# Kernel optimization log

Measured on AMD Instinct MI355X. Metric: run time of the kernel, lower is better.

Reference implementation:

```python
import jax, jax.numpy as jnp
import numpy as np

B, N, E = 4, 2048, 512
H = 8
HD = E // H  # 64
SCALE = HD ** -0.5


def setup_inputs() -> dict:
    key = jax.random.key(0)
    k1, k2, k3 = jax.random.split(key, 3)
    x = jax.random.normal(k1, (B, N, E), dtype=jnp.float32)
    # xavier-uniform-like scaling for weights
    w_qkv = jax.random.normal(k2, (3 * E, E), dtype=jnp.float32) * (2.0 / (4 * E)) ** 0.5
    b_qkv = jnp.zeros((3 * E,), dtype=jnp.float32)
    w_out = jax.random.normal(k3, (E, E), dtype=jnp.float32) * (1.0 / E) ** 0.5
    b_out = jnp.zeros((E,), dtype=jnp.float32)
    return {"x": x, "w_qkv": w_qkv, "b_qkv": b_qkv, "w_out": w_out, "b_out": b_out}


def reference(x, w_qkv, b_qkv, w_out, b_out):
    b_sz, n_patches, _ = x.shape
    # qkv projection: [B,N,3E] -> [B,N,3,H,HD] -> [B,H,3,N,HD]
    qkv = (jnp.einsum('bne,fe->bnf', x, w_qkv) + b_qkv)
    qkv = qkv.reshape(b_sz, n_patches, 3, H, HD).transpose(0, 3, 2, 1, 4)
    q, k, v = qkv[:, :, 0], qkv[:, :, 1], qkv[:, :, 2]  # each [B,H,N,HD]
    attn = jnp.einsum('bhqd,bhkd->bhqk', q * SCALE, k)  # [B,H,N,N]
    attn = jax.nn.softmax(attn, axis=-1)
    # attn_dropout p=0.0 -> identity in reference
    out = jnp.einsum('bhqk,bhkd->bhqd', attn, v)  # [B,H,N,HD]
    out = out.transpose(0, 2, 1, 3).reshape(b_sz, n_patches, E)
    out = jnp.einsum('bne,fe->bnf', out, w_out) + b_out
    return out
```

## Files before the change

kernel.cpp:

```cpp
#include <hip/hip_runtime.h>

#define BB   4
#define SEQ  2048
#define EMB  512
#define NH   8
#define HD   64
#define QSCALE 0.18033688011f

typedef __bf16 bf16x8 __attribute__((ext_vector_type(8)));
typedef float  f32x4  __attribute__((ext_vector_type(4)));

__device__ __forceinline__ short f2bf(float f) {
  union { float f; unsigned u; } v; v.f = f;
  unsigned r = v.u + 0x7fffu + ((v.u >> 16) & 1u);
  return (short)(r >> 16);
}

__device__ __forceinline__ unsigned pk_bf16(float a, float b) {
#if __has_builtin(__builtin_amdgcn_cvt_pk_bf16_f32)
  typedef __bf16 bf16v2 __attribute__((ext_vector_type(2)));
  union { bf16v2 v; unsigned u; } cv;
  cv.v = __builtin_amdgcn_cvt_pk_bf16_f32(a, b);
  return cv.u;
#else
  return (unsigned)(unsigned short)f2bf(a) | ((unsigned)(unsigned short)f2bf(b) << 16);
#endif
}

__device__ __forceinline__ float fexp2(float x) {
#if __has_builtin(__builtin_amdgcn_exp2f)
  return __builtin_amdgcn_exp2f(x);
#else
  return exp2f(x);
#endif
}

__device__ __forceinline__ void gl_lds16(const void* g, void* l) {
  __builtin_amdgcn_global_load_lds(
      (const __attribute__((address_space(1))) unsigned int*)g,
      (__attribute__((address_space(3))) unsigned int*)l, 16, 0, 0);
}

__device__ __forceinline__ void quad_redist(unsigned &a, unsigned &b) {
  asm volatile("v_permlane32_swap_b32 %0, %1" : "+v"(a), "+v"(b));
  asm volatile("v_permlane16_swap_b32 %0, %1" : "+v"(a), "+v"(b));
}

__global__ __launch_bounds__(256) void cast_all(const float* __restrict__ x,
                                                const float* __restrict__ wq,
                                                const float* __restrict__ wo,
                                                short* __restrict__ xb,
                                                short* __restrict__ wqb,
                                                short* __restrict__ wob) {
  int i = blockIdx.x * 256 + threadIdx.x;
  const float* src; short* dst; int off;
  if (i < 1048576)      { src = x;  dst = xb;  off = i; }
  else if (i < 1245184) { src = wq; dst = wqb; off = i - 1048576; }
  else                  { src = wo; dst = wob; off = i - 1245184; }
  float4 v = ((const float4*)src)[off];
  uint2 o; o.x = pk_bf16(v.x, v.y); o.y = pk_bf16(v.z, v.w);
  *(uint2*)&dst[off * 4] = o;
}

__global__ __launch_bounds__(256) void qkv_gemm(const short* __restrict__ A,
                                                const short* __restrict__ W,
                                                const float* __restrict__ bias,
                                                short* __restrict__ qo,
                                                short* __restrict__ ko,
                                                short* __restrict__ vto) {
  __shared__ __align__(16) short As0[128 * 32];
  __shared__ __align__(16) short Bs0[128 * 32];
  __shared__ __align__(16) short As1[128 * 32];
  __shared__ __align__(16) short Bs1[128 * 32];
  const int tid  = threadIdx.x;
  const int lane = tid & 63, wave = tid >> 6;
  const int wm = wave >> 1, wf = wave & 1;
  const int col = lane & 15, quad = lane >> 4;
  const int m0 = blockIdx.x * 128, f0 = blockIdx.y * 128;

  const short* aSrc[2]; const short* wSrc[2];
#pragma unroll
  for (int rd = 0; rd < 2; ++rd) {
    int slot = rd * 256 + tid;
    int row  = slot >> 2;
    int cb   = (slot & 3) ^ ((slot >> 3) & 3);
    aSrc[rd] = A + (size_t)(m0 + row) * 512 + cb * 8;
    wSrc[rd] = W + (size_t)(f0 + row) * 512 + cb * 8;
  }
  int aOff[4], bOff[4];
  const int rc = (quad ^ ((col >> 1) & 3)) * 8;
#pragma unroll
  for (int i = 0; i < 4; ++i) {
    aOff[i] = (wm * 64 + i * 16 + col) * 32 + rc;
    bOff[i] = (wf * 64 + i * 16 + col) * 32 + rc;
  }

  f32x4 acc[4][4];
#pragma unroll
  for (int i = 0; i < 4; ++i)
#pragma unroll
    for (int j = 0; j < 4; ++j)
#pragma unroll
      for (int r = 0; r < 4; ++r) acc[i][j][r] = 0.f;

#define QSTAGE(BUFA, BUFB, KS)                                         \
  {                                                                    \
    const int ko_ = (KS) * 32;                                         \
    gl_lds16(aSrc[0] + ko_, (char*)(BUFA) + wave * 1024);              \
    gl_lds16(aSrc[1] + ko_, (char*)(BUFA) + 4096 + wave * 1024);       \
    gl_lds16(wSrc[0] + ko_, (char*)(BUFB) + wave * 1024);              \
    gl_lds16(wSrc[1] + ko_, (char*)(BUFB) + 4096 + wave * 1024);       \
  }

  auto qcompute = [&](const short* As, const short* Bs) {
    bf16x8 af[4], bw[4];
#pragma unroll
    for (int i = 0; i < 4; ++i) af[i] = *(const bf16x8*)&As[aOff[i]];
#pragma unroll
    for (int j = 0; j < 4; ++j) bw[j] = *(const bf16x8*)&Bs[bOff[j]];
#pragma unroll
    for (int i = 0; i < 4; ++i)
#pragma unroll
      for (int j = 0; j < 4; ++j)
        acc[i][j] = __builtin_amdgcn_mfma_f32_16x16x32_bf16(af[i], bw[j], acc[i][j], 0, 0, 0);
  };

  QSTAGE(As0, Bs0, 0);
  __syncthreads();
  for (int t = 0; t < 16; t += 2) {
    QSTAGE(As1, Bs1, t + 1);
    qcompute(As0, Bs0);
    __syncthreads();
    QSTAGE(As0, Bs0, (t + 2) & 15);
    qcompute(As1, Bs1);
    __syncthreads();
  }
#undef QSTAGE

#pragma unroll
  for (int j = 0; j < 4; ++j) {
    const int f = f0 + wf * 64 + j * 16 + col;
    const float bv = bias[f];
    const int sIdx = f >> 9;
    const int h = (f >> 6) & 7;
    const int d = f & 63;
#pragma unroll
    for (int i = 0; i < 4; ++i) {
      const int mbase = m0 + wm * 64 + i * 16 + quad * 4;
      const int b = mbase >> 11;
      const int n = mbase & 2047;
      const size_t bh = (size_t)(b * NH + h);
      if (sIdx == 2) {
        uint2 pk;
        pk.x = pk_bf16(acc[i][j][0] + bv, acc[i][j][1] + bv);
        pk.y = pk_bf16(acc[i][j][2] + bv, acc[i][j][3] + bv);
        *(uint2*)&vto[(bh * HD + d) * SEQ + n] = pk;
      } else if (sIdx == 0) {
#pragma unroll
        for (int r = 0; r < 4; ++r)
          qo[(bh * SEQ + n + r) * HD + d] = f2bf((acc[i][j][r] + bv) * QSCALE);
      } else {
#pragma unroll
        for (int r = 0; r < 4; ++r)
          ko[(bh * SEQ + n + r) * HD + d] = f2bf(acc[i][j][r] + bv);
      }
    }
  }
}

__global__ __launch_bounds__(512) void attn_kernel(const short* __restrict__ q,
                                                   const short* __restrict__ k,
                                                   const short* __restrict__ vt,
                                                   short* __restrict__ o) {
  __shared__ __align__(16) short Ks0[64 * 64];
  __shared__ __align__(16) short Vs0[64 * 64];
  __shared__ __align__(16) short Ks1[64 * 64];
  __shared__ __align__(16) short Vs1[64 * 64];

  const int tid  = threadIdx.x;
  const int lane = tid & 63, wave = tid >> 6;
  const int col = lane & 15, quad = lane >> 4;
  const int bh = blockIdx.x & 31;
  const int q0 = (blockIdx.x >> 5) * 128;
  const size_t bhBase = (size_t)bh * SEQ * HD;

  bf16x8 qf[2];
#pragma unroll
  for (int ks = 0; ks < 2; ++ks)
    qf[ks] = *(const bf16x8*)&q[bhBase +
        (size_t)(q0 + wave * 16 + col) * HD + ks * 32 + quad * 8];

  const int row = tid >> 3, cb = (tid & 7) ^ (row & 7);
  const short* ksrc = k  + bhBase + (size_t)row * HD  + cb * 8;
  const short* vsrc = vt + bhBase + (size_t)row * SEQ + cb * 8;
  char* const ldsK0 = (char*)Ks0 + wave * 1024;
  char* const ldsV0 = (char*)Vs0 + wave * 1024;
  char* const ldsK1 = (char*)Ks1 + wave * 1024;
  char* const ldsV1 = (char*)Vs1 + wave * 1024;

  f32x4 oacc[4];
#pragma unroll
  for (int nt = 0; nt < 4; ++nt)
#pragma unroll
    for (int r = 0; r < 4; ++r) oacc[nt][r] = 0.f;
  float lsum = 0.f;

  auto compute = [&](const short* KB, const short* VB) {
    f32x4 sacc[4];
#pragma unroll
    for (int kt = 0; kt < 4; ++kt)
#pragma unroll
      for (int r = 0; r < 4; ++r) sacc[kt][r] = 0.f;
#pragma unroll
    for (int ks = 0; ks < 2; ++ks)
#pragma unroll
      for (int kt = 0; kt < 4; ++kt) {
        bf16x8 kf = *(const bf16x8*)&KB[(kt * 16 + col) * 64 +
                                        (((ks * 4 + quad) ^ (col & 7)) * 8)];
        sacc[kt] = __builtin_amdgcn_mfma_f32_16x16x32_bf16(kf, qf[ks], sacc[kt], 0, 0, 0);
      }

    unsigned u[4][2];
#pragma unroll
    for (int kt = 0; kt < 4; ++kt) {
      float p0 = fexp2(sacc[kt][0]);
      float p1 = fexp2(sacc[kt][1]);
      float p2 = fexp2(sacc[kt][2]);
      float p3 = fexp2(sacc[kt][3]);
      lsum += (p0 + p1) + (p2 + p3);
      u[kt][0] = pk_bf16(p0, p1);
      u[kt][1] = pk_bf16(p2, p3);
    }

    union { unsigned w[4]; bf16x8 v; } pf0, pf1;
    {
      unsigned a, b;
      a = u[0][0]; b = u[1][0]; quad_redist(a, b); pf0.w[0] = a; pf0.w[2] = b;
      a = u[0][1]; b = u[1][1]; quad_redist(a, b); pf0.w[1] = a; pf0.w[3] = b;
      a = u[2][0]; b = u[3][0]; quad_redist(a, b); pf1.w[0] = a; pf1.w[2] = b;
      a = u[2][1]; b = u[3][1]; quad_redist(a, b); pf1.w[1] = a; pf1.w[3] = b;
    }

#pragma unroll
    for (int nt = 0; nt < 4; ++nt) {
      bf16x8 vf0 = *(const bf16x8*)&VB[(nt * 16 + col) * 64 +
                                       ((quad ^ (col & 7)) * 8)];
      oacc[nt] = __builtin_amdgcn_mfma_f32_16x16x32_bf16(pf0.v, vf0, oacc[nt], 0, 0, 0);
      bf16x8 vf1 = *(const bf16x8*)&VB[(nt * 16 + col) * 64 +
                                       (((4 + quad) ^ (col & 7)) * 8)];
      oacc[nt] = __builtin_amdgcn_mfma_f32_16x16x32_bf16(pf1.v, vf1, oacc[nt], 0, 0, 0);
    }
  };

  gl_lds16(ksrc, ldsK0); gl_lds16(vsrc, ldsV0);
  ksrc += 64 * HD; vsrc += 64;
  __syncthreads();

  for (int t = 0; t < 32; t += 2) {
    gl_lds16(ksrc, ldsK1); gl_lds16(vsrc, ldsV1);
    ksrc += 64 * HD; vsrc += 64;
    compute(Ks0, Vs0);
    __syncthreads();
    gl_lds16(ksrc, ldsK0); gl_lds16(vsrc, ldsV0);
    ksrc += 64 * HD; vsrc += 64;
    compute(Ks1, Vs1);
    __syncthreads();
  }

  lsum += __shfl_xor(lsum, 16);
  lsum += __shfl_xor(lsum, 32);

  const int b = bh >> 3, h = bh & 7;
#pragma unroll
  for (int r = 0; r < 4; ++r) {
    const float rl = 1.0f / __shfl(lsum, quad * 4 + r);
    const int n = q0 + wave * 16 + quad * 4 + r;
#pragma unroll
    for (int nt = 0; nt < 4; ++nt)
      o[((size_t)(b * SEQ + n)) * EMB + h * HD + nt * 16 + col] = f2bf(oacc[nt][r] * rl);
  }
}

__global__ __launch_bounds__(256) void proj_gemm(const short* __restrict__ A,
                                                 const short* __restrict__ W,
                                                 const float* __restrict__ bias,
                                                 float* __restrict__ out) {
  __shared__ __align__(16) short As0[64 * 32];
  __shared__ __align__(16) short Bs0[128 * 32];
  __shared__ __align__(16) short As1[64 * 32];
  __shared__ __align__(16) short Bs1[128 * 32];
  const int tid  = threadIdx.x;
  const int lane = tid & 63, wave = tid >> 6;
  const int wm = wave >> 1, wf = wave & 1;
  const int col = lane & 15, quad = lane >> 4;
  const int m0 = blockIdx.x * 64, f0 = blockIdx.y * 128;

  const short* aSrcP;
  {
    int row = tid >> 2;
    int cb  = (tid & 3) ^ ((tid >> 3) & 3);
    aSrcP = A + (size_t)(m0 + row) * 512 + cb * 8;
  }
  const short* wSrcP[2];
#pragma unroll
  for (int rd = 0; rd < 2; ++rd) {
    int slot = rd * 256 + tid;
    int row  = slot >> 2;
    int cb   = (slot & 3) ^ ((slot >> 3) & 3);
    wSrcP[rd] = W + (size_t)(f0 + row) * 512 + cb * 8;
  }
  int aOff[2], bOff[4];
  const int rc = (quad ^ ((col >> 1) & 3)) * 8;
#pragma unroll
  for (int i = 0; i < 2; ++i)
    aOff[i] = (wm * 32 + i * 16 + col) * 32 + rc;
#pragma unroll
  for (int j = 0; j < 4; ++j)
    bOff[j] = (wf * 64 + j * 16 + col) * 32 + rc;

  f32x4 acc[2][4];
#pragma unroll
  for (int i = 0; i < 2; ++i)
#pragma unroll
    for (int j = 0; j < 4; ++j)
#pragma unroll
      for (int r = 0; r < 4; ++r) acc[i][j][r] = 0.f;

#define PSTAGE(BUFA, BUFB, KS)                                         \
  {                                                                    \
    const int ko_ = (KS) * 32;                                         \
    gl_lds16(aSrcP + ko_, (char*)(BUFA) + wave * 1024);                \
    gl_lds16(wSrcP[0] + ko_, (char*)(BUFB) + wave * 1024);             \
    gl_lds16(wSrcP[1] + ko_, (char*)(BUFB) + 4096 + wave * 1024);      \
  }

  auto pcompute = [&](const short* As, const short* Bs) {
    bf16x8 af[2], bw[4];
#pragma unroll
    for (int i = 0; i < 2; ++i) af[i] = *(const bf16x8*)&As[aOff[i]];
#pragma unroll
    for (int j = 0; j < 4; ++j) bw[j] = *(const bf16x8*)&Bs[bOff[j]];
#pragma unroll
    for (int i = 0; i < 2; ++i)
#pragma unroll
      for (int j = 0; j < 4; ++j)
        acc[i][j] = __builtin_amdgcn_mfma_f32_16x16x32_bf16(af[i], bw[j], acc[i][j], 0, 0, 0);
  };

  PSTAGE(As0, Bs0, 0);
  __syncthreads();
  for (int t = 0; t < 16; t += 2) {
    PSTAGE(As1, Bs1, t + 1);
    pcompute(As0, Bs0);
    __syncthreads();
    PSTAGE(As0, Bs0, (t + 2) & 15);
    pcompute(As1, Bs1);
    __syncthreads();
  }
#undef PSTAGE

#pragma unroll
  for (int j = 0; j < 4; ++j) {
    const int f = f0 + wf * 64 + j * 16 + col;
    const float bv = bias[f];
#pragma unroll
    for (int i = 0; i < 2; ++i) {
      const int mbase = m0 + wm * 32 + i * 16 + quad * 4;
#pragma unroll
      for (int r = 0; r < 4; ++r)
        out[(size_t)(mbase + r) * 512 + f] = acc[i][j][r] + bv;
    }
  }
}

extern "C" void kernel_launch(void* const* d_in, const int* in_sizes, int n_in,
                              void* d_out, int out_size, void* d_ws, size_t ws_size,
                              hipStream_t stream) {
  (void)in_sizes; (void)n_in; (void)out_size; (void)ws_size;
  const float* x     = (const float*)d_in[0];
  const float* w_qkv = (const float*)d_in[1];
  const float* b_qkv = (const float*)d_in[2];
  const float* w_out = (const float*)d_in[3];
  const float* b_out = (const float*)d_in[4];
  float* out = (float*)d_out;

  char* ws = (char*)d_ws;
  short* xb    = (short*)(ws + 0);
  short* wqkvb = (short*)(ws + 8388608);
  short* woutb = (short*)(ws + 9961472);
  short* qb    = (short*)(ws + 10485760);
  short* kb    = (short*)(ws + 18874368);
  short* vtb   = (short*)(ws + 27262976);
  short* ob    = (short*)(ws + 35651584);

  cast_all<<<5120, 256, 0, stream>>>(x, w_qkv, w_out, xb, wqkvb, woutb);
  qkv_gemm<<<dim3(64, 12), 256, 0, stream>>>(xb, wqkvb, b_qkv, qb, kb, vtb);
  attn_kernel<<<512, 512, 0, stream>>>(qb, kb, vtb, ob);
  proj_gemm<<<dim3(128, 4), 256, 0, stream>>>(ob, woutb, b_out, out);
}
```

Baseline: 162.7 us.

## Fuse fp32-to-bf16 casts into GEMM operand loading, drop cast kernel

Removes the separate cast_all kernel. qkv_gemm now reads fp32 x and w_qkv from global memory into registers, converts them to bf16 and writes them into the swizzled LDS tiles. proj_gemm does the same for w_out. This removes one launch and the round trip of the bf16 copies through memory. In exchange the GEMMs read twice as many bytes per operand, lose the async global_load_lds path for those operands, and use more registers for the staged data.

```diff
diff --git a/kernel.cpp b/kernel.cpp
--- a/kernel.cpp
+++ b/kernel.cpp
@@ -46,24 +46,15 @@
   asm volatile("v_permlane16_swap_b32 %0, %1" : "+v"(a), "+v"(b));
 }
 
-__global__ __launch_bounds__(256) void cast_all(const float* __restrict__ x,
-                                                const float* __restrict__ wq,
-                                                const float* __restrict__ wo,
-                                                short* __restrict__ xb,
-                                                short* __restrict__ wqb,
-                                                short* __restrict__ wob) {
-  int i = blockIdx.x * 256 + threadIdx.x;
-  const float* src; short* dst; int off;
-  if (i < 1048576)      { src = x;  dst = xb;  off = i; }
-  else if (i < 1245184) { src = wq; dst = wqb; off = i - 1048576; }
-  else                  { src = wo; dst = wob; off = i - 1245184; }
-  float4 v = ((const float4*)src)[off];
-  uint2 o; o.x = pk_bf16(v.x, v.y); o.y = pk_bf16(v.z, v.w);
-  *(uint2*)&dst[off * 4] = o;
-}
-
-__global__ __launch_bounds__(256) void qkv_gemm(const short* __restrict__ A,
-                                                const short* __restrict__ W,
+__device__ __forceinline__ uint4 cast8(const float4 a, const float4 b) {
+  uint4 w;
+  w.x = pk_bf16(a.x, a.y); w.y = pk_bf16(a.z, a.w);
+  w.z = pk_bf16(b.x, b.y); w.w = pk_bf16(b.z, b.w);
+  return w;
+}
+
+__global__ __launch_bounds__(256) void qkv_gemm(const float* __restrict__ X,
+                                                const float* __restrict__ W,
                                                 const float* __restrict__ bias,
                                                 short* __restrict__ qo,
                                                 short* __restrict__ ko,
@@ -78,14 +69,16 @@
   const int col = lane & 15, quad = lane >> 4;
   const int m0 = blockIdx.x * 128, f0 = blockIdx.y * 128;
 
-  const short* aSrc[2]; const short* wSrc[2];
+  const float* aS[2]; const float* wS[2];
+  int dstOff[2];
 #pragma unroll
   for (int rd = 0; rd < 2; ++rd) {
     int slot = rd * 256 + tid;
     int row  = slot >> 2;
     int cb   = (slot & 3) ^ ((slot >> 3) & 3);
-    aSrc[rd] = A + (size_t)(m0 + row) * 512 + cb * 8;
-    wSrc[rd] = W + (size_t)(f0 + row) * 512 + cb * 8;
+    aS[rd] = X + (size_t)(m0 + row) * 512 + cb * 8;
+    wS[rd] = W + (size_t)(f0 + row) * 512 + cb * 8;
+    dstOff[rd] = slot * 16;
   }
   int aOff[4], bOff[4];
   const int rc = (quad ^ ((col >> 1) & 3)) * 8;
@@ -103,13 +96,26 @@
 #pragma unroll
       for (int r = 0; r < 4; ++r) acc[i][j][r] = 0.f;
 
-#define QSTAGE(BUFA, BUFB, KS)                                         \
-  {                                                                    \
-    const int ko_ = (KS) * 32;                                         \
-    gl_lds16(aSrc[0] + ko_, (char*)(BUFA) + wave * 1024);              \
-    gl_lds16(aSrc[1] + ko_, (char*)(BUFA) + 4096 + wave * 1024);       \
-    gl_lds16(wSrc[0] + ko_, (char*)(BUFB) + wave * 1024);              \
-    gl_lds16(wSrc[1] + ko_, (char*)(BUFB) + 4096 + wave * 1024);       \
+  float4 ra[2][2], rw[2][2];
+
+#define QLOAD(KS)                                                       \
+  {                                                                     \
+    const int ko_ = (KS) * 32;                                          \
+    _Pragma("unroll")                                                   \
+    for (int rd = 0; rd < 2; ++rd) {                                    \
+      ra[rd][0] = *(const float4*)(aS[rd] + ko_);                       \
+      ra[rd][1] = *(const float4*)(aS[rd] + ko_ + 4);                   \
+      rw[rd][0] = *(const float4*)(wS[rd] + ko_);                       \
+      rw[rd][1] = *(const float4*)(wS[rd] + ko_ + 4);                   \
+    }                                                                   \
+  }
+#define QWRITE(BUFA, BUFB)                                              \
+  {                                                                     \
+    _Pragma("unroll")                                                   \
+    for (int rd = 0; rd < 2; ++rd) {                                    \
+      *(uint4*)((char*)(BUFA) + dstOff[rd]) = cast8(ra[rd][0], ra[rd][1]); \
+      *(uint4*)((char*)(BUFB) + dstOff[rd]) = cast8(rw[rd][0], rw[rd][1]); \
+    }                                                                   \
   }
 
   auto qcompute = [&](const short* As, const short* Bs) {
@@ -125,17 +131,20 @@
         acc[i][j] = __builtin_amdgcn_mfma_f32_16x16x32_bf16(af[i], bw[j], acc[i][j], 0, 0, 0);
   };
 
-  QSTAGE(As0, Bs0, 0);
+  QLOAD(0); QWRITE(As0, Bs0);
   __syncthreads();
   for (int t = 0; t < 16; t += 2) {
-    QSTAGE(As1, Bs1, t + 1);
+    QLOAD(t + 1);
     qcompute(As0, Bs0);
-    __syncthreads();
-    QSTAGE(As0, Bs0, (t + 2) & 15);
+    QWRITE(As1, Bs1);
+    __syncthreads();
+    QLOAD((t + 2) & 15);
     qcompute(As1, Bs1);
-    __syncthreads();
-  }
-#undef QSTAGE
+    QWRITE(As0, Bs0);
+    __syncthreads();
+  }
+#undef QLOAD
+#undef QWRITE
 
 #pragma unroll
   for (int j = 0; j < 4; ++j) {
@@ -282,7 +291,7 @@
 }
 
 __global__ __launch_bounds__(256) void proj_gemm(const short* __restrict__ A,
-                                                 const short* __restrict__ W,
+                                                 const float* __restrict__ W,
                                                  const float* __restrict__ bias,
                                                  float* __restrict__ out) {
   __shared__ __align__(16) short As0[64 * 32];
@@ -301,13 +310,15 @@
     int cb  = (tid & 3) ^ ((tid >> 3) & 3);
     aSrcP = A + (size_t)(m0 + row) * 512 + cb * 8;
   }
-  const short* wSrcP[2];
+  const float* wS[2];
+  int dstOff[2];
 #pragma unroll
   for (int rd = 0; rd < 2; ++rd) {
     int slot = rd * 256 + tid;
     int row  = slot >> 2;
     int cb   = (slot & 3) ^ ((slot >> 3) & 3);
-    wSrcP[rd] = W + (size_t)(f0 + row) * 512 + cb * 8;
+    wS[rd] = W + (size_t)(f0 + row) * 512 + cb * 8;
+    dstOff[rd] = slot * 16;
   }
   int aOff[2], bOff[4];
   const int rc = (quad ^ ((col >> 1) & 3)) * 8;
@@ -326,13 +337,25 @@
 #pragma unroll
       for (int r = 0; r < 4; ++r) acc[i][j][r] = 0.f;
 
-#define PSTAGE(BUFA, BUFB, KS)                                         \
-  {                                                                    \
-    const int ko_ = (KS) * 32;                                         \
-    gl_lds16(aSrcP + ko_, (char*)(BUFA) + wave * 1024);                \
-    gl_lds16(wSrcP[0] + ko_, (char*)(BUFB) + wave * 1024);             \
-    gl_lds16(wSrcP[1] + ko_, (char*)(BUFB) + 4096 + wave * 1024);      \
-  }
+  float4 rw[2][2];
+
+#define PLOADW(KS)                                                      \
+  {                                                                     \
+    const int ko_ = (KS) * 32;                                          \
+    _Pragma("unroll")                                                   \
+    for (int rd = 0; rd < 2; ++rd) {                                    \
+      rw[rd][0] = *(const float4*)(wS[rd] + ko_);                       \
+      rw[rd][1] = *(const float4*)(wS[rd] + ko_ + 4);                   \
+    }                                                                   \
+  }
+#define PWRITEW(BUFB)                                                   \
+  {                                                                     \
+    _Pragma("unroll")                                                   \
+    for (int rd = 0; rd < 2; ++rd)                                      \
+      *(uint4*)((char*)(BUFB) + dstOff[rd]) = cast8(rw[rd][0], rw[rd][1]); \
+  }
+#define PLOADA(BUFA, KS)                                                \
+    gl_lds16(aSrcP + (KS) * 32, (char*)(BUFA) + wave * 1024);
 
   auto pcompute = [&](const short* As, const short* Bs) {
     bf16x8 af[2], bw[4];
@@ -347,17 +370,23 @@
         acc[i][j] = __builtin_amdgcn_mfma_f32_16x16x32_bf16(af[i], bw[j], acc[i][j], 0, 0, 0);
   };
 
-  PSTAGE(As0, Bs0, 0);
+  PLOADW(0); PWRITEW(Bs0); PLOADA(As0, 0);
   __syncthreads();
   for (int t = 0; t < 16; t += 2) {
-    PSTAGE(As1, Bs1, t + 1);
+    PLOADA(As1, t + 1);
+    PLOADW(t + 1);
     pcompute(As0, Bs0);
-    __syncthreads();
-    PSTAGE(As0, Bs0, (t + 2) & 15);
+    PWRITEW(Bs1);
+    __syncthreads();
+    PLOADA(As0, (t + 2) & 15);
+    PLOADW((t + 2) & 15);
     pcompute(As1, Bs1);
-    __syncthreads();
-  }
-#undef PSTAGE
+    PWRITEW(Bs0);
+    __syncthreads();
+  }
+#undef PLOADW
+#undef PWRITEW
+#undef PLOADA
 
 #pragma unroll
   for (int j = 0; j < 4; ++j) {
@@ -385,16 +414,12 @@
   float* out = (float*)d_out;
 
   char* ws = (char*)d_ws;
-  short* xb    = (short*)(ws + 0);
-  short* wqkvb = (short*)(ws + 8388608);
-  short* woutb = (short*)(ws + 9961472);
-  short* qb    = (short*)(ws + 10485760);
-  short* kb    = (short*)(ws + 18874368);
-  short* vtb   = (short*)(ws + 27262976);
-  short* ob    = (short*)(ws + 35651584);
-
-  cast_all<<<5120, 256, 0, stream>>>(x, w_qkv, w_out, xb, wqkvb, woutb);
-  qkv_gemm<<<dim3(64, 12), 256, 0, stream>>>(xb, wqkvb, b_qkv, qb, kb, vtb);
+  short* qb  = (short*)(ws + 0);
+  short* kb  = (short*)(ws + 8388608);
+  short* vtb = (short*)(ws + 16777216);
+  short* ob  = (short*)(ws + 25165824);
+
+  qkv_gemm<<<dim3(64, 12), 256, 0, stream>>>(x, w_qkv, b_qkv, qb, kb, vtb);
   attn_kernel<<<512, 512, 0, stream>>>(qb, kb, vtb, ob);
-  proj_gemm<<<dim3(128, 4), 256, 0, stream>>>(ob, woutb, b_out, out);
-}
+  proj_gemm<<<dim3(128, 4), 256, 0, stream>>>(ob, w_out, b_out, out);
+}
```

New measurement: 199.7 us. 22.7% more time.
